# Optimization experiments

Measured on AMD Instinct MI355X. Metric: run time of the kernel, lower is better.

The kernel has to match this reference:

```python
import jax, jax.numpy as jnp
import numpy as np

N, C, K, H = 131072, 512, 128, 8  # points, channels, patch_size, heads


def setup_inputs() -> dict:
    key = jax.random.key(0)
    ks = jax.random.split(key, 6)
    feat = jax.random.normal(ks[0], (N, C), dtype=jnp.float32)
    Wqkv = jax.random.normal(ks[1], (C, 3 * C), dtype=jnp.float32) * 0.02
    bqkv = jax.random.normal(ks[2], (3 * C,), dtype=jnp.float32) * 0.02
    Wproj = jax.random.normal(ks[3], (C, C), dtype=jnp.float32) * 0.02
    bproj = jax.random.normal(ks[4], (C,), dtype=jnp.float32) * 0.02
    order = jax.random.permutation(ks[5], N).astype(jnp.int64)  # serialized order (all clusters full)
    inverse = jnp.argsort(order).astype(jnp.int64)              # serialized inverse
    return {"feat": feat, "Wqkv": Wqkv, "bqkv": bqkv, "Wproj": Wproj,
            "bproj": bproj, "order": order, "inverse": inverse}


def reference(feat, Wqkv, bqkv, Wproj, bproj, order, inverse):
    hd = C // H
    scale = hd ** -0.5
    qkv = feat @ Wqkv + bqkv                 # [N, 3C]
    qkv = qkv[order]                         # gather by serialized order
    qkv = qkv.reshape(-1, K, 3, H, hd)       # [W, K, 3, H, hd]
    qkv = jnp.moveaxis(qkv, 2, 0)            # [3, W, K, H, hd]
    q = jnp.swapaxes(qkv[0], 1, 2)           # [W, H, K, hd]
    k = jnp.swapaxes(qkv[1], 1, 2)
    v = jnp.swapaxes(qkv[2], 1, 2)
    # upcast_attention / upcast_softmax -> compute scores & softmax in fp32
    attn = jnp.einsum('whkd,whjd->whkj', (q * scale).astype(jnp.float32),
                      k.astype(jnp.float32))             # [W, H, K, K]
    attn = jax.nn.softmax(attn, axis=-1).astype(feat.dtype)
    out = jnp.einsum('whkj,whjd->whkd', attn, v)          # [W, H, K, hd]
    out = jnp.swapaxes(out, 1, 2).reshape(-1, C)          # [N, C]
    out = out[inverse]                                    # scatter back via inverse
    out = out @ Wproj + bproj
    return out
```

## Files before the change

### kernel.cpp

```cpp
#include <hip/hip_runtime.h>
#include <hip/hip_bf16.h>
#include <cstdint>
#include <cstddef>

typedef __bf16 bf16;
typedef __bf16 bf16x8 __attribute__((ext_vector_type(8)));
typedef float f32x4 __attribute__((ext_vector_type(4)));

#define N_PTS 131072
#define CDIM  512
#define C3    1536
#define HD    64
#define NH    8
#define KWIN  128

static __device__ __forceinline__ bf16 cvt(float x) { return (bf16)x; }

static __device__ __forceinline__ void gld16(const bf16* g, bf16* l) {
    __builtin_amdgcn_global_load_lds(
        (const __attribute__((address_space(1))) void*)g,
        (__attribute__((address_space(3))) void*)l, 16, 0, 0);
}

__global__ __launch_bounds__(256) void k_prep(
    const float* __restrict__ Wqkv, const float* __restrict__ Wproj,
    bf16* __restrict__ Wqkv_t, bf16* __restrict__ Wproj_t)
{
    int idx = blockIdx.x * 256 + threadIdx.x;
    if (idx < CDIM * C3) {
        int k = idx / C3, c = idx % C3;
        Wqkv_t[(size_t)c * CDIM + k] = cvt(Wqkv[idx]);
    } else {
        int j = idx - CDIM * C3;
        if (j < CDIM * CDIM) {
            int k = j / CDIM, c = j % CDIM;
            Wproj_t[(size_t)c * CDIM + k] = cvt(Wproj[j]);
        }
    }
}

__global__ __launch_bounds__(256) void k_gather(
    const float* __restrict__ feat, const int* __restrict__ order,
    bf16* __restrict__ feat_g)
{
    int row = blockIdx.x * 2 + (threadIdx.x >> 7);
    int c   = (threadIdx.x & 127) << 2;
    int src = order[row];
    float4 v = *reinterpret_cast<const float4*>(feat + (size_t)src * CDIM + c);
    union { bf16 e[4]; uint2 u; } pk;
    pk.e[0] = cvt(v.x); pk.e[1] = cvt(v.y); pk.e[2] = cvt(v.z); pk.e[3] = cvt(v.w);
    *reinterpret_cast<uint2*>(feat_g + (size_t)row * CDIM + c) = pk.u;
}

template <bool F32OUT, int NT>
__global__ __launch_bounds__(512) void k_gemm(
    const bf16* __restrict__ Ag, const bf16* __restrict__ Bt,
    const float* __restrict__ bias, void* __restrict__ outp)
{
    __shared__ __align__(16) bf16 As[4][256 * 32];
    __shared__ __align__(16) bf16 Bs[4][256 * 32];

    const int t    = threadIdx.x;
    const int lane = t & 63;
    const int wv   = t >> 6;
    const int wr   = wv >> 2;
    const int wc   = wv & 3;
    const int g    = lane >> 4, r16 = lane & 15;

    const int nwg = gridDim.x;
    const int bid = blockIdx.x;
    const int swz = (bid & 7) * (nwg >> 3) + (bid >> 3);
    const int m0  = (swz / NT) * 256;
    const int n0  = (swz % NT) * 256;

    const int L0 = wv * 64 + lane;
    const int L1 = L0 + 512;
    const int r0 = L0 >> 2, s0 = ((L0 & 3) - (r0 >> 1)) & 3;
    const int r1 = L1 >> 2, s1 = ((L1 & 3) - (r1 >> 1)) & 3;
    const bf16* sA0 = Ag + (size_t)(m0 + r0) * CDIM + s0 * 8;
    const bf16* sA1 = Ag + (size_t)(m0 + r1) * CDIM + s1 * 8;
    const bf16* sB0 = Bt + (size_t)(n0 + r0) * CDIM + s0 * 8;
    const bf16* sB1 = Bt + (size_t)(n0 + r1) * CDIM + s1 * 8;

    int aoff[8], boff[4];
#pragma unroll
    for (int i = 0; i < 8; ++i) {
        int row = wr * 128 + i * 16 + r16;
        aoff[i] = row * 64 + (((g + (row >> 1)) & 3) << 4);
    }
#pragma unroll
    for (int n = 0; n < 4; ++n) {
        int row = wc * 64 + n * 16 + r16;
        boff[n] = row * 64 + (((g + (row >> 1)) & 3) << 4);
    }

    f32x4 acc[8][4];
    const f32x4 z = {0.f, 0.f, 0.f, 0.f};
#pragma unroll
    for (int i = 0; i < 8; ++i)
#pragma unroll
        for (int n = 0; n < 4; ++n) acc[i][n] = z;

    auto stage = [&](int kt) {
        const int b  = kt & 3;
        const int ko = kt * 32;
        gld16(sA0 + ko, &As[b][(size_t)wv * 64 * 8]);
        gld16(sA1 + ko, &As[b][(size_t)(512 + wv * 64) * 8]);
        gld16(sB0 + ko, &Bs[b][(size_t)wv * 64 * 8]);
        gld16(sB1 + ko, &Bs[b][(size_t)(512 + wv * 64) * 8]);
    };

    auto compute = [&](int kt) {
        const int b = kt & 3;
        bf16x8 af[8], bv[4];
#pragma unroll
        for (int i = 0; i < 8; ++i)
            af[i] = *reinterpret_cast<const bf16x8*>(
                reinterpret_cast<const char*>(&As[b][0]) + aoff[i]);
#pragma unroll
        for (int n = 0; n < 4; ++n)
            bv[n] = *reinterpret_cast<const bf16x8*>(
                reinterpret_cast<const char*>(&Bs[b][0]) + boff[n]);
        __builtin_amdgcn_s_setprio(1);
#pragma unroll
        for (int i = 0; i < 8; ++i)
#pragma unroll
            for (int n = 0; n < 4; ++n)
                acc[i][n] = __builtin_amdgcn_mfma_f32_16x16x32_bf16(
                    af[i], bv[n], acc[i][n], 0, 0, 0);
        __builtin_amdgcn_s_setprio(0);
    };

    stage(0); stage(1); stage(2);
    asm volatile("s_waitcnt vmcnt(8)" ::: "memory");
    __builtin_amdgcn_s_barrier();

#pragma unroll
    for (int kt = 0; kt < 13; ++kt) {
        stage(kt + 3);
        compute(kt);
        asm volatile("s_waitcnt vmcnt(8) lgkmcnt(0)" ::: "memory");
        __builtin_amdgcn_s_barrier();
    }
    compute(13);
    asm volatile("s_waitcnt vmcnt(4) lgkmcnt(0)" ::: "memory");
    __builtin_amdgcn_s_barrier();
    compute(14);
    asm volatile("s_waitcnt vmcnt(0) lgkmcnt(0)" ::: "memory");
    __builtin_amdgcn_s_barrier();
    compute(15);

    const int ldo = NT * 256;
#pragma unroll
    for (int n = 0; n < 4; ++n) {
        int col = n0 + wc * 64 + n * 16 + r16;
        float b = bias[col];
#pragma unroll
        for (int i = 0; i < 8; ++i)
#pragma unroll
            for (int j = 0; j < 4; ++j) {
                int row = m0 + wr * 128 + i * 16 + g * 4 + j;
                if (F32OUT)
                    reinterpret_cast<float*>(outp)[(size_t)row * ldo + col] =
                        acc[i][n][j] + b;
                else
                    reinterpret_cast<bf16*>(outp)[(size_t)row * ldo + col] =
                        cvt(acc[i][n][j] + b);
            }
    }
}

__global__ __launch_bounds__(256) void k_attn(
    const bf16* __restrict__ qkv_s, const int* __restrict__ order,
    bf16* __restrict__ attn_g)
{
    __shared__ __align__(16) char smem[36864 + 64 * 136 * 2];
    __shared__ int ord_s[KWIN];
    bf16 (*Q)[72]   = reinterpret_cast<bf16 (*)[72]>(smem);
    bf16 (*Kt)[72]  = reinterpret_cast<bf16 (*)[72]>(smem + 128 * 72 * 2);
    bf16 (*P)[136]  = reinterpret_cast<bf16 (*)[136]>(smem);
    bf16 (*Vt)[136] = reinterpret_cast<bf16 (*)[136]>(smem + 36864);

    const int t    = threadIdx.x;
    const int lane = t & 63;
    const int wv   = t >> 6;
    const int g    = lane >> 4, r16 = lane & 15;
    const int h    = blockIdx.x;
    const int w    = blockIdx.y;

    const bf16* base = qkv_s + (size_t)w * KWIN * C3 + h * HD;

    if (t < KWIN) ord_s[t] = order[w * KWIN + t];

#pragma unroll
    for (int it = 0; it < 4; ++it) {
        int s   = it * 256 + t;
        int tok = s >> 3;
        int c8  = (s & 7) << 3;
        size_t roff = (size_t)tok * C3 + c8;
        *reinterpret_cast<uint4*>(&Q[tok][c8])  =
            *reinterpret_cast<const uint4*>(base + roff);
        *reinterpret_cast<uint4*>(&Kt[tok][c8]) =
            *reinterpret_cast<const uint4*>(base + roff + CDIM);
        uint4 vvec = *reinterpret_cast<const uint4*>(base + roff + 2 * CDIM);
        const bf16* ve = reinterpret_cast<const bf16*>(&vvec);
#pragma unroll
        for (int i = 0; i < 8; ++i) Vt[c8 + i][tok] = ve[i];
    }
    __syncthreads();

    f32x4 sc[2][8];
    const f32x4 z = {0.f, 0.f, 0.f, 0.f};
#pragma unroll
    for (int m = 0; m < 2; ++m)
#pragma unroll
        for (int n = 0; n < 8; ++n) sc[m][n] = z;

#pragma unroll
    for (int ks = 0; ks < 2; ++ks) {
        bf16x8 aq[2];
#pragma unroll
        for (int m = 0; m < 2; ++m)
            aq[m] = *reinterpret_cast<const bf16x8*>(
                &Q[wv * 32 + m * 16 + r16][ks * 32 + g * 8]);
#pragma unroll
        for (int n = 0; n < 8; ++n) {
            bf16x8 bk = *reinterpret_cast<const bf16x8*>(
                &Kt[n * 16 + r16][ks * 32 + g * 8]);
#pragma unroll
            for (int m = 0; m < 2; ++m)
                sc[m][n] = __builtin_amdgcn_mfma_f32_16x16x32_bf16(
                    aq[m], bk, sc[m][n], 0, 0, 0);
        }
    }

    const float scale = 0.125f;
    float inv_sum[2][4];
#pragma unroll
    for (int m = 0; m < 2; ++m) {
#pragma unroll
        for (int j = 0; j < 4; ++j) {
            float mx = -3.0e38f;
#pragma unroll
            for (int n = 0; n < 8; ++n) mx = fmaxf(mx, sc[m][n][j]);
            mx = fmaxf(mx, __shfl_xor(mx, 1));
            mx = fmaxf(mx, __shfl_xor(mx, 2));
            mx = fmaxf(mx, __shfl_xor(mx, 4));
            mx = fmaxf(mx, __shfl_xor(mx, 8));
            mx *= scale;
            float ssum = 0.f;
#pragma unroll
            for (int n = 0; n < 8; ++n) {
                float p = __expf(sc[m][n][j] * scale - mx);
                sc[m][n][j] = p;
                ssum += p;
            }
            ssum += __shfl_xor(ssum, 1);
            ssum += __shfl_xor(ssum, 2);
            ssum += __shfl_xor(ssum, 4);
            ssum += __shfl_xor(ssum, 8);
            inv_sum[m][j] = 1.f / ssum;
        }
    }

    __syncthreads();

#pragma unroll
    for (int m = 0; m < 2; ++m)
#pragma unroll
        for (int n = 0; n < 8; ++n)
#pragma unroll
            for (int j = 0; j < 4; ++j)
                P[wv * 32 + m * 16 + g * 4 + j][n * 16 + r16] =
                    cvt(sc[m][n][j] * inv_sum[m][j]);

    f32x4 o[2][4];
#pragma unroll
    for (int m = 0; m < 2; ++m)
#pragma unroll
        for (int n = 0; n < 4; ++n) o[m][n] = z;

#pragma unroll
    for (int kt = 0; kt < 4; ++kt) {
        bf16x8 ap[2];
#pragma unroll
        for (int m = 0; m < 2; ++m)
            ap[m] = *reinterpret_cast<const bf16x8*>(
                &P[wv * 32 + m * 16 + r16][kt * 32 + g * 8]);
#pragma unroll
        for (int n = 0; n < 4; ++n) {
            bf16x8 bv = *reinterpret_cast<const bf16x8*>(
                &Vt[n * 16 + r16][kt * 32 + g * 8]);
#pragma unroll
            for (int m = 0; m < 2; ++m)
                o[m][n] = __builtin_amdgcn_mfma_f32_16x16x32_bf16(
                    ap[m], bv, o[m][n], 0, 0, 0);
        }
    }

#pragma unroll
    for (int m = 0; m < 2; ++m)
#pragma unroll
        for (int n = 0; n < 4; ++n)
#pragma unroll
            for (int j = 0; j < 4; ++j) {
                int tok  = wv * 32 + m * 16 + g * 4 + j;
                int d    = n * 16 + r16;
                int drow = ord_s[tok];
                attn_g[(size_t)drow * CDIM + h * HD + d] = cvt(o[m][n][j]);
            }
}

extern "C" void kernel_launch(void* const* d_in, const int* in_sizes, int n_in,
                              void* d_out, int out_size, void* d_ws, size_t ws_size,
                              hipStream_t stream)
{
    const float* feat    = (const float*)d_in[0];
    const float* Wqkv    = (const float*)d_in[1];
    const float* bqkv    = (const float*)d_in[2];
    const float* Wproj   = (const float*)d_in[3];
    const float* bproj   = (const float*)d_in[4];
    const int*   order   = (const int*)d_in[5];
    float* out = (float*)d_out;

    const size_t qkv_bytes  = (size_t)N_PTS * C3 * sizeof(bf16);
    const size_t gat_bytes  = (size_t)N_PTS * CDIM * sizeof(bf16);
    const size_t wq_bytes   = (size_t)C3 * CDIM * sizeof(bf16);
    const size_t wp_bytes   = (size_t)CDIM * CDIM * sizeof(bf16);
    if (ws_size < qkv_bytes + gat_bytes + wq_bytes + wp_bytes) return;

    bf16* qkv_s     = (bf16*)d_ws;
    bf16* shared134 = (bf16*)((char*)d_ws + qkv_bytes);
    bf16* Wqkv_t    = (bf16*)((char*)d_ws + qkv_bytes + gat_bytes);
    bf16* Wproj_t   = (bf16*)((char*)d_ws + qkv_bytes + gat_bytes + wq_bytes);

    k_prep<<<dim3((CDIM * C3 + CDIM * CDIM + 255) / 256), 256, 0, stream>>>(
        Wqkv, Wproj, Wqkv_t, Wproj_t);
    k_gather<<<dim3(N_PTS / 2), 256, 0, stream>>>(feat, order, shared134);
    k_gemm<false, C3 / 256><<<dim3((N_PTS / 256) * (C3 / 256)), 512, 0, stream>>>(
        shared134, Wqkv_t, bqkv, qkv_s);
    k_attn<<<dim3(NH, N_PTS / KWIN), 256, 0, stream>>>(qkv_s, order, shared134);
    k_gemm<true, CDIM / 256><<<dim3((N_PTS / 256) * (CDIM / 256)), 512, 0, stream>>>(
        shared134, Wproj_t, bproj, out);
}
```

Before: 656.5 us.

## Shrink GEMM tile to 128x256 with double buffering for higher occupancy

The bf16 GEMM kernel changes its tile from 256x256 with a 4-stage LDS pipeline to 128x256 with a 2-stage pipeline. This cuts accumulator registers and LDS per block, and launch_bounds(512,4) asks for more resident blocks to hide latency. In exchange the loads sit behind an extra barrier per k-step, so there is less prefetch depth, and each block reuses less data with more B reloads.

```diff
diff --git a/kernel.cpp b/kernel.cpp
--- a/kernel.cpp
+++ b/kernel.cpp
@@ -53,12 +53,12 @@
 }
 
 template <bool F32OUT, int NT>
-__global__ __launch_bounds__(512) void k_gemm(
+__global__ __launch_bounds__(512, 4) void k_gemm(
     const bf16* __restrict__ Ag, const bf16* __restrict__ Bt,
     const float* __restrict__ bias, void* __restrict__ outp)
 {
-    __shared__ __align__(16) bf16 As[4][256 * 32];
-    __shared__ __align__(16) bf16 Bs[4][256 * 32];
+    __shared__ __align__(16) bf16 As[2][128 * 32];
+    __shared__ __align__(16) bf16 Bs[2][256 * 32];
 
     const int t    = threadIdx.x;
     const int lane = t & 63;
@@ -70,23 +70,21 @@
     const int nwg = gridDim.x;
     const int bid = blockIdx.x;
     const int swz = (bid & 7) * (nwg >> 3) + (bid >> 3);
-    const int m0  = (swz / NT) * 256;
+    const int m0  = (swz / NT) * 128;
     const int n0  = (swz % NT) * 256;
 
     const int L0 = wv * 64 + lane;
-    const int L1 = L0 + 512;
-    const int r0 = L0 >> 2, s0 = ((L0 & 3) - (r0 >> 1)) & 3;
-    const int r1 = L1 >> 2, s1 = ((L1 & 3) - (r1 >> 1)) & 3;
-    const bf16* sA0 = Ag + (size_t)(m0 + r0) * CDIM + s0 * 8;
-    const bf16* sA1 = Ag + (size_t)(m0 + r1) * CDIM + s1 * 8;
-    const bf16* sB0 = Bt + (size_t)(n0 + r0) * CDIM + s0 * 8;
-    const bf16* sB1 = Bt + (size_t)(n0 + r1) * CDIM + s1 * 8;
-
-    int aoff[8], boff[4];
-#pragma unroll
-    for (int i = 0; i < 8; ++i) {
-        int row = wr * 128 + i * 16 + r16;
-        aoff[i] = row * 64 + (((g + (row >> 1)) & 3) << 4);
+    const int rA = L0 >> 2,          sA = ((L0 & 3) - (rA >> 1)) & 3;
+    const int rB1 = rA + 128,        sB1v = ((L0 & 3) - (rB1 >> 1)) & 3;
+    const bf16* srcA  = Ag + (size_t)(m0 + rA) * CDIM + sA * 8;
+    const bf16* srcB0 = Bt + (size_t)(n0 + rA) * CDIM + sA * 8;
+    const bf16* srcB1 = Bt + (size_t)(n0 + rB1) * CDIM + sB1v * 8;
+
+    int aoff[4], boff[4];
+#pragma unroll
+    for (int m = 0; m < 4; ++m) {
+        int row = wr * 64 + m * 16 + r16;
+        aoff[m] = row * 64 + (((g + (row >> 1)) & 3) << 4);
     }
 #pragma unroll
     for (int n = 0; n < 4; ++n) {
@@ -94,61 +92,61 @@
         boff[n] = row * 64 + (((g + (row >> 1)) & 3) << 4);
     }
 
-    f32x4 acc[8][4];
+    f32x4 acc[4][4];
     const f32x4 z = {0.f, 0.f, 0.f, 0.f};
 #pragma unroll
-    for (int i = 0; i < 8; ++i)
-#pragma unroll
-        for (int n = 0; n < 4; ++n) acc[i][n] = z;
+    for (int m = 0; m < 4; ++m)
+#pragma unroll
+        for (int n = 0; n < 4; ++n) acc[m][n] = z;
 
     auto stage = [&](int kt) {
-        const int b  = kt & 3;
+        const int b  = kt & 1;
         const int ko = kt * 32;
-        gld16(sA0 + ko, &As[b][(size_t)wv * 64 * 8]);
-        gld16(sA1 + ko, &As[b][(size_t)(512 + wv * 64) * 8]);
-        gld16(sB0 + ko, &Bs[b][(size_t)wv * 64 * 8]);
-        gld16(sB1 + ko, &Bs[b][(size_t)(512 + wv * 64) * 8]);
+        gld16(srcA  + ko, &As[b][(size_t)wv * 64 * 8]);
+        gld16(srcB0 + ko, &Bs[b][(size_t)wv * 64 * 8]);
+        gld16(srcB1 + ko, &Bs[b][(size_t)(512 + wv * 64) * 8]);
     };
 
     auto compute = [&](int kt) {
-        const int b = kt & 3;
-        bf16x8 af[8], bv[4];
-#pragma unroll
-        for (int i = 0; i < 8; ++i)
-            af[i] = *reinterpret_cast<const bf16x8*>(
-                reinterpret_cast<const char*>(&As[b][0]) + aoff[i]);
+        const int b = kt & 1;
+        bf16x8 af[4], bv[4];
+#pragma unroll
+        for (int m = 0; m < 4; ++m)
+            af[m] = *reinterpret_cast<const bf16x8*>(
+                reinterpret_cast<const char*>(&As[b][0]) + aoff[m]);
 #pragma unroll
         for (int n = 0; n < 4; ++n)
             bv[n] = *reinterpret_cast<const bf16x8*>(
                 reinterpret_cast<const char*>(&Bs[b][0]) + boff[n]);
         __builtin_amdgcn_s_setprio(1);
 #pragma unroll
-        for (int i = 0; i < 8; ++i)
+        for (int m = 0; m < 4; ++m)
 #pragma unroll
             for (int n = 0; n < 4; ++n)
-                acc[i][n] = __builtin_amdgcn_mfma_f32_16x16x32_bf16(
-                    af[i], bv[n], acc[i][n], 0, 0, 0);
+                acc[m][n] = __builtin_amdgcn_mfma_f32_16x16x32_bf16(
+                    af[m], bv[n], acc[m][n], 0, 0, 0);
         __builtin_amdgcn_s_setprio(0);
     };
 
-    stage(0); stage(1); stage(2);
-    asm volatile("s_waitcnt vmcnt(8)" ::: "memory");
+    const int NKT = CDIM / 32;
+
+    stage(0); stage(1);
+    asm volatile("s_waitcnt vmcnt(3)" ::: "memory");
     __builtin_amdgcn_s_barrier();
 
 #pragma unroll
-    for (int kt = 0; kt < 13; ++kt) {
-        stage(kt + 3);
+    for (int kt = 0; kt < NKT - 2; ++kt) {
         compute(kt);
-        asm volatile("s_waitcnt vmcnt(8) lgkmcnt(0)" ::: "memory");
+        asm volatile("s_waitcnt lgkmcnt(0)" ::: "memory");
         __builtin_amdgcn_s_barrier();
-    }
-    compute(13);
-    asm volatile("s_waitcnt vmcnt(4) lgkmcnt(0)" ::: "memory");
-    __builtin_amdgcn_s_barrier();
-    compute(14);
+        stage(kt + 2);
+        asm volatile("s_waitcnt vmcnt(3)" ::: "memory");
+        __builtin_amdgcn_s_barrier();
+    }
+    compute(NKT - 2);
     asm volatile("s_waitcnt vmcnt(0) lgkmcnt(0)" ::: "memory");
     __builtin_amdgcn_s_barrier();
-    compute(15);
+    compute(NKT - 1);
 
     const int ldo = NT * 256;
 #pragma unroll
@@ -156,16 +154,16 @@
         int col = n0 + wc * 64 + n * 16 + r16;
         float b = bias[col];
 #pragma unroll
-        for (int i = 0; i < 8; ++i)
+        for (int m = 0; m < 4; ++m)
 #pragma unroll
             for (int j = 0; j < 4; ++j) {
-                int row = m0 + wr * 128 + i * 16 + g * 4 + j;
+                int row = m0 + wr * 64 + m * 16 + g * 4 + j;
                 if (F32OUT)
                     reinterpret_cast<float*>(outp)[(size_t)row * ldo + col] =
-                        acc[i][n][j] + b;
+                        acc[m][n][j] + b;
                 else
                     reinterpret_cast<bf16*>(outp)[(size_t)row * ldo + col] =
-                        cvt(acc[i][n][j] + b);
+                        cvt(acc[m][n][j] + b);
             }
     }
 }
@@ -337,9 +335,9 @@
     k_prep<<<dim3((CDIM * C3 + CDIM * CDIM + 255) / 256), 256, 0, stream>>>(
         Wqkv, Wproj, Wqkv_t, Wproj_t);
     k_gather<<<dim3(N_PTS / 2), 256, 0, stream>>>(feat, order, shared134);
-    k_gemm<false, C3 / 256><<<dim3((N_PTS / 256) * (C3 / 256)), 512, 0, stream>>>(
+    k_gemm<false, C3 / 256><<<dim3((N_PTS / 128) * (C3 / 256)), 512, 0, stream>>>(
         shared134, Wqkv_t, bqkv, qkv_s);
     k_attn<<<dim3(NH, N_PTS / KWIN), 256, 0, stream>>>(qkv_s, order, shared134);
-    k_gemm<true, CDIM / 256><<<dim3((N_PTS / 256) * (CDIM / 256)), 512, 0, stream>>>(
+    k_gemm<true, CDIM / 256><<<dim3((N_PTS / 128) * (CDIM / 256)), 512, 0, stream>>>(
         shared134, Wproj_t, bproj, out);
 }
```

Result: faster. 640.1 us (-2.5%).
